# Kernel optimization log

Measured on AMD Instinct MI355X. Metric: run time of the kernel, lower is better.

Reference implementation:

```python
import jax, jax.numpy as jnp
import numpy as np

N = 50000
E = 800000
D = 256   # output_channel_dim
K = 32
L = 4     # num_of_layers


def setup_inputs() -> dict:
    key = jax.random.key(0)
    ks = jax.random.split(key, 10)
    x = jax.random.normal(ks[0], (N, 1), dtype=jnp.float32)
    edge_index = jax.random.randint(ks[1], (2, E), 0, N, dtype=jnp.int64)
    edge_attr = jax.random.uniform(ks[2], (E,), dtype=jnp.float32)
    # GGNN per-layer propagation weights (L, D, D)
    weight = jax.random.normal(ks[3], (L, D, D), dtype=jnp.float32) / np.sqrt(D)
    # GRUCell params (torch layout: [r|z|n] stacked along first dim)
    w_ih = jax.random.normal(ks[4], (3 * D, D), dtype=jnp.float32) / np.sqrt(D)
    w_hh = jax.random.normal(ks[5], (3 * D, D), dtype=jnp.float32) / np.sqrt(D)
    b_ih = jax.random.normal(ks[6], (3 * D,), dtype=jnp.float32) * 0.01
    b_hh = jax.random.normal(ks[7], (3 * D,), dtype=jnp.float32) * 0.01
    # readout Linear(D, K)
    w_ro = jax.random.normal(ks[8], (D, K), dtype=jnp.float32) / np.sqrt(D)
    b_ro = jax.random.normal(ks[9], (K,), dtype=jnp.float32) * 0.01
    return {"x": x, "edge_index": edge_index, "edge_attr": edge_attr,
            "weight": weight, "w_ih": w_ih, "w_hh": w_hh,
            "b_ih": b_ih, "b_hh": b_hh, "w_ro": w_ro, "b_ro": b_ro}


def _gru_cell(m, h, w_ih, w_hh, b_ih, b_hh):
    # torch.nn.GRUCell math; gates stacked [r|z|n]
    gi = m @ w_ih.T + b_ih   # (N, 3D)
    gh = h @ w_hh.T + b_hh   # (N, 3D)
    i_r, i_z, i_n = jnp.split(gi, 3, axis=-1)
    h_r, h_z, h_n = jnp.split(gh, 3, axis=-1)
    r = jax.nn.sigmoid(i_r + h_r)
    z = jax.nn.sigmoid(i_z + h_z)
    n = jnp.tanh(i_n + r * h_n)
    return (1.0 - z) * n + z * h


def reference(x, edge_index, edge_attr, weight, w_ih, w_hh, b_ih, b_hh, w_ro, b_ro):
    src, dst = edge_index[0], edge_index[1]
    n_nodes, d = x.shape[0], weight.shape[-1]
    # pad input features with zeros up to out_channels
    h = jnp.concatenate([x, jnp.zeros((n_nodes, d - x.shape[-1]), x.dtype)], axis=-1)
    for i in range(weight.shape[0]):
        m = h @ weight[i]                                    # (N, D)
        msg = edge_attr[:, None] * m[src]                    # (E, D)
        agg = jax.ops.segment_sum(msg, dst, num_segments=n_nodes)  # (N, D)
        h = _gru_cell(agg, h, w_ih, w_hh, b_ih, b_hh)
    logits = h @ w_ro + b_ro                                 # (N, K)
    return jax.nn.softmax(logits, axis=-1)
```

## Files before the change

### kernel.cpp

```cpp
#include <hip/hip_runtime.h>

#define D 256
#define K_OUT 32
#define L_LAYERS 4
#define NPAD 50048

typedef __attribute__((ext_vector_type(8))) short bf16x8;
typedef __attribute__((ext_vector_type(4))) float f32x4;
typedef __attribute__((address_space(3))) unsigned int lds_u32;
typedef const __attribute__((address_space(1))) unsigned int glb_u32;

__device__ __forceinline__ float sigm(float v) { return 1.f / (1.f + __expf(-v)); }
__device__ __forceinline__ unsigned short f2bf(float f) {
    unsigned u = __float_as_uint(f);
    u = u + 0x7fffu + ((u >> 16) & 1u);
    return (unsigned short)(u >> 16);
}
__device__ __forceinline__ float bf2f(unsigned short s) {
    return __uint_as_float(((unsigned)s) << 16);
}
__device__ __forceinline__ void gload16(const unsigned short* g, unsigned short* l) {
    __builtin_amdgcn_global_load_lds((glb_u32*)g, (lds_u32*)l, 16, 0, 0);
}

__global__ __launch_bounds__(256) void hist_kernel(const int* __restrict__ dst,
                                                   int* __restrict__ cnt, int E) {
    int idx = blockIdx.x * blockDim.x + threadIdx.x;
    for (int e = idx; e < E; e += gridDim.x * blockDim.x)
        atomicAdd(&cnt[dst[e]], 1);
}

__global__ __launch_bounds__(1024) void scan_kernel(const int* __restrict__ cnt,
                                                    int* __restrict__ rowptr,
                                                    int* __restrict__ cursor, int n) {
    __shared__ int sdata[1024];
    int t = threadIdx.x;
    int chunk = (n + 1023) / 1024;
    int start = t * chunk;
    int end = start + chunk; if (end > n) end = n;
    int s = 0;
    for (int i = start; i < end; i++) s += cnt[i];
    sdata[t] = s;
    __syncthreads();
    for (int off = 1; off < 1024; off <<= 1) {
        int v = (t >= off) ? sdata[t - off] : 0;
        __syncthreads();
        sdata[t] += v;
        __syncthreads();
    }
    int base = sdata[t] - s;
    for (int i = start; i < end; i++) {
        rowptr[i] = base;
        cursor[i] = base;
        base += cnt[i];
    }
    if (end == n && start <= n) rowptr[n] = base;
}

__global__ __launch_bounds__(256) void reorder_kernel(const int* __restrict__ src,
                                                      const int* __restrict__ dst,
                                                      const float* __restrict__ ea,
                                                      int* __restrict__ cursor,
                                                      int* __restrict__ esrc,
                                                      float* __restrict__ eval, int E) {
    int idx = blockIdx.x * blockDim.x + threadIdx.x;
    for (int e = idx; e < E; e += gridDim.x * blockDim.x) {
        int slot = atomicAdd(&cursor[dst[e]], 1);
        esrc[slot] = src[e];
        eval[slot] = ea[e];
    }
}

__global__ __launch_bounds__(256) void prep_wih_kernel(const float* __restrict__ weight,
                                                       const float* __restrict__ w_ih,
                                                       float* __restrict__ P) {
    int l = blockIdx.z;
    const float* A = weight + (size_t)l * D * D;
    float* Cdst = P + (size_t)l * 256 * 768;
    __shared__ float As[32][64 + 4];
    __shared__ float Bs[32][64 + 4];
    int tid = threadIdx.x;
    int tx = tid & 15, ty = tid >> 4;
    int bk = blockIdx.x * 64;
    int bn = blockIdx.y * 64;
    float acc[4][4] = {};
    for (int jb = 0; jb < D; jb += 32) {
        #pragma unroll
        for (int i = 0; i < 2; i++) {
            int lin = tid + i * 256;
            int row = lin >> 3;
            int c4 = (lin & 7) << 2;
            float4 v = *(const float4*)&A[(size_t)(bk + row) * D + jb + c4];
            As[c4+0][row]=v.x; As[c4+1][row]=v.y; As[c4+2][row]=v.z; As[c4+3][row]=v.w;
            float4 w = *(const float4*)&w_ih[(size_t)(bn + row) * D + jb + c4];
            Bs[c4+0][row]=w.x; Bs[c4+1][row]=w.y; Bs[c4+2][row]=w.z; Bs[c4+3][row]=w.w;
        }
        __syncthreads();
        #pragma unroll
        for (int jj = 0; jj < 32; jj++) {
            float a[4], b[4];
            *(float4*)a = *(const float4*)&As[jj][ty*4];
            *(float4*)b = *(const float4*)&Bs[jj][tx*4];
            #pragma unroll
            for (int i = 0; i < 4; i++)
                #pragma unroll
                for (int j = 0; j < 4; j++)
                    acc[i][j] += a[i] * b[j];
        }
        __syncthreads();
    }
    #pragma unroll
    for (int i = 0; i < 4; i++)
        *(float4*)&Cdst[(size_t)(bk + ty*4 + i) * 768 + bn + tx*4] =
            make_float4(acc[i][0], acc[i][1], acc[i][2], acc[i][3]);
}

__global__ __launch_bounds__(256) void pack_bt2_kernel(const float* __restrict__ P,
                                                       const float* __restrict__ w_hh,
                                                       unsigned short* __restrict__ BT2) {
    long long idx = (long long)blockIdx.x * 256 + threadIdx.x;
    int l = (int)(idx >> 20);
    int rem = (int)(idx & 1048575);
    int c = rem >> 10;
    int k2 = rem & 1023;
    int g = c >> 8, d = c & 255;
    int k = k2 & 511;
    float val;
    if (k < 256) {
        val = (g == 0) ? P[(size_t)l * 196608 + (size_t)k * 768 + d]
            : (g == 1) ? P[(size_t)l * 196608 + (size_t)k * 768 + 256 + d]
            : (g == 2) ? P[(size_t)l * 196608 + (size_t)k * 768 + 512 + d]
            : 0.f;
    } else {
        int kk = k - 256;
        val = (g == 0) ? w_hh[(size_t)d * D + kk]
            : (g == 1) ? w_hh[(size_t)(256 + d) * D + kk]
            : (g == 3) ? w_hh[(size_t)(512 + d) * D + kk]
            : 0.f;
    }
    unsigned short hi = f2bf(val);
    BT2[idx] = (k2 < 512) ? hi : f2bf(val - bf2f(hi));
}

__global__ __launch_bounds__(256) void sgather_kernel(const float* __restrict__ x,
                                                      const int* __restrict__ rowptr,
                                                      const int* __restrict__ esrc,
                                                      const float* __restrict__ eval,
                                                      float* __restrict__ sx, int n) {
    int node = blockIdx.x * blockDim.x + threadIdx.x;
    if (node >= n) return;
    float s = 0.f;
    int end = rowptr[node + 1];
    for (int e = rowptr[node]; e < end; e++) s += eval[e] * x[esrc[e]];
    sx[node] = s;
}

__global__ __launch_bounds__(256) void layer0_kernel(const float* __restrict__ x,
                                                     const float* __restrict__ sx,
                                                     const float* __restrict__ P0,
                                                     const float* __restrict__ w_hh,
                                                     const float* __restrict__ b_ih,
                                                     const float* __restrict__ b_hh,
                                                     float* __restrict__ hout, int M) {
    int node = blockIdx.x * 4 + (threadIdx.x >> 6);
    if (node >= M) return;
    int d0 = (threadIdx.x & 63) * 4;
    float sxn = sx[node], xn = x[node];
    float4 r0 = *(const float4*)&P0[d0];
    float4 z0 = *(const float4*)&P0[256 + d0];
    float4 n0 = *(const float4*)&P0[512 + d0];
    float r1[4], z1[4], n1[4];
    #pragma unroll
    for (int j = 0; j < 4; j++) {
        r1[j] = w_hh[(size_t)(d0 + j) * D];
        z1[j] = w_hh[(size_t)(256 + d0 + j) * D];
        n1[j] = w_hh[(size_t)(512 + d0 + j) * D];
    }
    float4 bir = *(const float4*)&b_ih[d0];
    float4 biz = *(const float4*)&b_ih[256 + d0];
    float4 bin = *(const float4*)&b_ih[512 + d0];
    float4 bhr = *(const float4*)&b_hh[d0];
    float4 bhz = *(const float4*)&b_hh[256 + d0];
    float4 bhn = *(const float4*)&b_hh[512 + d0];
    float rr[4] = {sxn*r0.x + xn*r1[0] + bir.x + bhr.x, sxn*r0.y + xn*r1[1] + bir.y + bhr.y,
                   sxn*r0.z + xn*r1[2] + bir.z + bhr.z, sxn*r0.w + xn*r1[3] + bir.w + bhr.w};
    float zz[4] = {sxn*z0.x + xn*z1[0] + biz.x + bhz.x, sxn*z0.y + xn*z1[1] + biz.y + bhz.y,
                   sxn*z0.z + xn*z1[2] + biz.z + bhz.z, sxn*z0.w + xn*z1[3] + biz.w + bhz.w};
    float ni[4] = {sxn*n0.x + bin.x, sxn*n0.y + bin.y, sxn*n0.z + bin.z, sxn*n0.w + bin.w};
    float nh[4] = {xn*n1[0] + bhn.x, xn*n1[1] + bhn.y, xn*n1[2] + bhn.z, xn*n1[3] + bhn.w};
    float o[4];
    #pragma unroll
    for (int j = 0; j < 4; j++) {
        float r = sigm(rr[j]);
        float z = sigm(zz[j]);
        float nn = tanhf(ni[j] + r * nh[j]);
        float hp = (d0 + j == 0) ? xn : 0.f;
        o[j] = (1.f - z) * nn + z * hp;
    }
    *(float4*)&hout[(size_t)node * D + d0] = make_float4(o[0], o[1], o[2], o[3]);
}

__global__ __launch_bounds__(256) void gather_bf_kernel(const float* __restrict__ h,
                                                        const int* __restrict__ rowptr,
                                                        const int* __restrict__ esrc,
                                                        const float* __restrict__ eval,
                                                        unsigned short* __restrict__ A2, int n) {
    int node = (blockIdx.x * 256 + threadIdx.x) >> 6;
    int lane = threadIdx.x & 63;
    if (node >= n) return;
    int beg = rowptr[node], end = rowptr[node + 1];
    float4 acc = make_float4(0.f, 0.f, 0.f, 0.f);
    for (int e = beg; e < end; e++) {
        int s = esrc[e];
        float a = eval[e];
        float4 v = *(const float4*)&h[(size_t)s * D + lane * 4];
        acc.x += a * v.x; acc.y += a * v.y; acc.z += a * v.z; acc.w += a * v.w;
    }
    ushort4 hi = make_ushort4(f2bf(acc.x), f2bf(acc.y), f2bf(acc.z), f2bf(acc.w));
    ushort4 lo = make_ushort4(f2bf(acc.x - bf2f(hi.x)), f2bf(acc.y - bf2f(hi.y)),
                              f2bf(acc.z - bf2f(hi.z)), f2bf(acc.w - bf2f(hi.w)));
    *(ushort4*)&A2[(size_t)node * 1024 + lane * 4] = hi;
    *(ushort4*)&A2[(size_t)node * 1024 + 512 + lane * 4] = lo;
    float4 hv = *(const float4*)&h[(size_t)node * D + lane * 4];
    ushort4 hh = make_ushort4(f2bf(hv.x), f2bf(hv.y), f2bf(hv.z), f2bf(hv.w));
    ushort4 hl = make_ushort4(f2bf(hv.x - bf2f(hh.x)), f2bf(hv.y - bf2f(hh.y)),
                              f2bf(hv.z - bf2f(hh.z)), f2bf(hv.w - bf2f(hh.w)));
    *(ushort4*)&A2[(size_t)node * 1024 + 256 + lane * 4] = hh;
    *(ushort4*)&A2[(size_t)node * 1024 + 768 + lane * 4] = hl;
}

__global__ __launch_bounds__(256, 2) void gru_mfma_kernel(const unsigned short* __restrict__ A2,
                                                          const unsigned short* __restrict__ BT2,
                                                          const float* __restrict__ b_ih,
                                                          const float* __restrict__ b_hh,
                                                          float* __restrict__ h, int M) {
    __shared__ unsigned short sm[24576];
    int tid = threadIdx.x;
    int lane = tid & 63;
    int wid = tid >> 6;
    int wr = wid >> 1, wc = wid & 1;
    int bm = blockIdx.x * 128;
    int bnd = blockIdx.y * 64;

    unsigned goff[12];
    bool gisA[12];
    #pragma unroll
    for (int ff = 0; ff < 12; ff++) {
        int f = wid * 12 + ff;
        unsigned r, cb;
        bool isA = (f < 16);
        if (f < 8)       { r = bm + f * 16 + (lane & 15);       cb = 0; }
        else if (f < 16) { r = bm + (f - 8) * 16 + (lane & 15); cb = 512; }
        else if (f < 32) { int q = f - 16; r = (q >> 2) * 256 + bnd + (q & 3) * 16 + (lane & 15); cb = 0; }
        else             { int q = f - 32; r = (q >> 2) * 256 + bnd + (q & 3) * 16 + (lane & 15); cb = 512; }
        goff[ff] = r * 1024u + cb + ((lane >> 4) << 3);
        gisA[ff] = isA;
    }

    f32x4 acc[4][8];
    #pragma unroll
    for (int i = 0; i < 4; i++)
        #pragma unroll
        for (int j = 0; j < 8; j++)
            acc[i][j] = (f32x4){0.f, 0.f, 0.f, 0.f};

    for (int c = 0; c < 16; c++) {
        #pragma unroll
        for (int ff = 0; ff < 12; ff++) {
            const unsigned short* g = (gisA[ff] ? A2 : BT2) + goff[ff] + c * 32;
            gload16(g, &sm[(wid * 12 + ff) * 512]);
        }
        __syncthreads();
        bf16x8 ah[4], al[4], bh[8], bl[8];
        #pragma unroll
        for (int m = 0; m < 4; m++) {
            ah[m] = *(const bf16x8*)&sm[(wr * 4 + m) * 512 + lane * 8];
            al[m] = *(const bf16x8*)&sm[(8 + wr * 4 + m) * 512 + lane * 8];
        }
        #pragma unroll
        for (int n = 0; n < 8; n++) {
            int fb = (n >> 1) * 4 + wc * 2 + (n & 1);
            bh[n] = *(const bf16x8*)&sm[(16 + fb) * 512 + lane * 8];
            bl[n] = *(const bf16x8*)&sm[(32 + fb) * 512 + lane * 8];
        }
        #pragma unroll
        for (int m = 0; m < 4; m++)
            #pragma unroll
            for (int n = 0; n < 8; n++) {
                acc[m][n] = __builtin_amdgcn_mfma_f32_16x16x32_bf16(ah[m], bh[n], acc[m][n], 0, 0, 0);
                acc[m][n] = __builtin_amdgcn_mfma_f32_16x16x32_bf16(al[m], bh[n], acc[m][n], 0, 0, 0);
                acc[m][n] = __builtin_amdgcn_mfma_f32_16x16x32_bf16(ah[m], bl[n], acc[m][n], 0, 0, 0);
            }
        __syncthreads();
    }

    int dbase = bnd + wc * 32 + (lane & 15);
    int rbase = bm + wr * 64 + ((lane >> 4) << 2);
    #pragma unroll
    for (int j = 0; j < 2; j++) {
        int d = dbase + j * 16;
        float cbr = b_ih[d] + b_hh[d];
        float cbz = b_ih[D + d] + b_hh[D + d];
        float bin = b_ih[2 * D + d];
        float bhn = b_hh[2 * D + d];
        #pragma unroll
        for (int m = 0; m < 4; m++) {
            #pragma unroll
            for (int q = 0; q < 4; q++) {
                int row = rbase + m * 16 + q;
                if (row < M) {
                    float r = sigm(acc[m][j][q] + cbr);
                    float z = sigm(acc[m][2 + j][q] + cbz);
                    float nn = tanhf(acc[m][4 + j][q] + bin + r * (acc[m][6 + j][q] + bhn));
                    float* hp = &h[(size_t)row * D + d];
                    float hv = *hp;
                    *hp = (1.f - z) * nn + z * hv;
                }
            }
        }
    }
}

__global__ __launch_bounds__(256) void readout_kernel(const float* __restrict__ h,
                                                      const float* __restrict__ w_ro,
                                                      const float* __restrict__ b_ro,
                                                      float* __restrict__ out, int M) {
    __shared__ float ws_[D * K_OUT];
    for (int i = threadIdx.x; i < D * K_OUT; i += 256) ws_[i] = w_ro[i];
    __syncthreads();
    int group = threadIdx.x >> 5;
    int col   = threadIdx.x & 31;
    int node  = blockIdx.x * 8 + group;
    if (node >= M) return;
    float acc = b_ro[col];
    const float* hrow = &h[(size_t)node * D];
    #pragma unroll 8
    for (int k = 0; k < D; k++) acc += hrow[k] * ws_[k * K_OUT + col];
    float mx = acc;
    #pragma unroll
    for (int off = 16; off > 0; off >>= 1) mx = fmaxf(mx, __shfl_xor(mx, off, 32));
    float e = __expf(acc - mx);
    float s = e;
    #pragma unroll
    for (int off = 16; off > 0; off >>= 1) s += __shfl_xor(s, off, 32);
    out[(size_t)node * K_OUT + col] = e / s;
}

extern "C" void kernel_launch(void* const* d_in, const int* in_sizes, int n_in,
                              void* d_out, int out_size, void* d_ws, size_t ws_size,
                              hipStream_t stream) {
    const float* x      = (const float*)d_in[0];
    const int*   ei     = (const int*)d_in[1];
    const float* ea     = (const float*)d_in[2];
    const float* weight = (const float*)d_in[3];
    const float* w_ih   = (const float*)d_in[4];
    const float* w_hh   = (const float*)d_in[5];
    const float* b_ih   = (const float*)d_in[6];
    const float* b_hh   = (const float*)d_in[7];
    const float* w_ro   = (const float*)d_in[8];
    const float* b_ro   = (const float*)d_in[9];
    float* out = (float*)d_out;

    int N = in_sizes[0];
    int E = in_sizes[2];
    const int* src = ei;
    const int* dst = ei + E;

    size_t ND = (size_t)N * D;
    float* h = (float*)d_ws;
    unsigned short* A2 = (unsigned short*)(h + ND);
    float* P = (float*)(A2 + (size_t)NPAD * 1024);
    unsigned short* BT2 = (unsigned short*)(P + (size_t)L_LAYERS * 256 * 768);
    float* sx = (float*)(BT2 + (size_t)L_LAYERS * 1024 * 1024);
    int* cnt = (int*)(sx + N);
    int* rowptr = cnt + (N + 1);
    int* cursor = rowptr + (N + 1);
    int* esrc = cursor + (N + 1);
    float* eval = (float*)(esrc + E);

    hipMemsetAsync(cnt, 0, (N + 1) * sizeof(int), stream);
    hist_kernel<<<1024, 256, 0, stream>>>(dst, cnt, E);
    scan_kernel<<<1, 1024, 0, stream>>>(cnt, rowptr, cursor, N);
    reorder_kernel<<<1024, 256, 0, stream>>>(src, dst, ea, cursor, esrc, eval, E);

    prep_wih_kernel<<<dim3(4, 12, 4), 256, 0, stream>>>(weight, w_ih, P);
    pack_bt2_kernel<<<16384, 256, 0, stream>>>(P, w_hh, BT2);

    sgather_kernel<<<(N + 255) / 256, 256, 0, stream>>>(x, rowptr, esrc, eval, sx, N);
    layer0_kernel<<<(N + 3) / 4, 256, 0, stream>>>(x, sx, P, w_hh, b_ih, b_hh, h, N);

    dim3 gm(NPAD / 128, 4);
    int gather_blocks = (N * 64 + 255) / 256;
    for (int l = 1; l < L_LAYERS; l++) {
        gather_bf_kernel<<<gather_blocks, 256, 0, stream>>>(h, rowptr, esrc, eval, A2, N);
        gru_mfma_kernel<<<gm, 256, 0, stream>>>(A2, BT2 + (size_t)l * 1024 * 1024,
                                                b_ih, b_hh, h, N);
    }
    readout_kernel<<<(N + 7) / 8, 256, 0, stream>>>(h, w_ro, b_ro, out, N);
}
```

Baseline: 1.605 ms.

## Double-buffer GRU GEMM LDS tiles and skip zero blocks of n-gate weights

The GRU MFMA kernel now double-buffers its LDS tiles, prefetching the next K-chunk while computing the current one, and drops one of the two barriers per iteration. It also exploits the block structure of the concatenated [agg|h] weight matrix: for the n gate, the first half of K uses only the input-side weights and the second half only the hidden-side weights. So it loads 6 instead of 8 B fragments per chunk and issues a quarter fewer MFMAs. LDS per block grows (2x20480 shorts), which could affect occupancy at launch bounds of 2.

After: 1.478 ms. 7.9% less time.

```diff
diff --git a/kernel.cpp b/kernel.cpp
--- a/kernel.cpp
+++ b/kernel.cpp
@@ -234,7 +234,7 @@
                                                           const float* __restrict__ b_ih,
                                                           const float* __restrict__ b_hh,
                                                           float* __restrict__ h, int M) {
-    __shared__ unsigned short sm[24576];
+    __shared__ unsigned short sm[2][20480];
     int tid = threadIdx.x;
     int lane = tid & 63;
     int wid = tid >> 6;
@@ -242,19 +242,21 @@
     int bm = blockIdx.x * 128;
     int bnd = blockIdx.y * 64;
 
-    unsigned goff[12];
-    bool gisA[12];
-    #pragma unroll
-    for (int ff = 0; ff < 12; ff++) {
-        int f = wid * 12 + ff;
-        unsigned r, cb;
-        bool isA = (f < 16);
-        if (f < 8)       { r = bm + f * 16 + (lane & 15);       cb = 0; }
-        else if (f < 16) { r = bm + (f - 8) * 16 + (lane & 15); cb = 512; }
-        else if (f < 32) { int q = f - 16; r = (q >> 2) * 256 + bnd + (q & 3) * 16 + (lane & 15); cb = 0; }
-        else             { int q = f - 32; r = (q >> 2) * 256 + bnd + (q & 3) * 16 + (lane & 15); cb = 512; }
-        goff[ff] = r * 1024u + cb + ((lane >> 4) << 3);
-        gisA[ff] = isA;
+    unsigned gbase[10];
+    bool gA[10], gG2[10];
+    #pragma unroll
+    for (int ff = 0; ff < 10; ff++) {
+        int f = wid * 10 + ff;
+        unsigned row, cb;
+        bool isA, isG2 = false;
+        if (f < 8)       { row = bm + f * 16 + (lane & 15);        cb = 0;   isA = true; }
+        else if (f < 16) { row = bm + (f - 8) * 16 + (lane & 15);  cb = 512; isA = true; }
+        else if (f < 28) { int q = f - 16; int gs = q >> 2; int df = q & 3;
+                           row = gs * 256 + bnd + df * 16 + (lane & 15); cb = 0; isA = false; isG2 = (gs == 2); }
+        else             { int q = f - 28; int gs = q >> 2; int df = q & 3;
+                           row = gs * 256 + bnd + df * 16 + (lane & 15); cb = 512; isA = false; isG2 = (gs == 2); }
+        gbase[ff] = row * 1024u + cb + ((lane >> 4) << 3);
+        gA[ff] = isA; gG2[ff] = isG2;
     }
 
     f32x4 acc[4][8];
@@ -264,41 +266,58 @@
         for (int j = 0; j < 8; j++)
             acc[i][j] = (f32x4){0.f, 0.f, 0.f, 0.f};
 
-    for (int c = 0; c < 16; c++) {
-        #pragma unroll
-        for (int ff = 0; ff < 12; ff++) {
-            const unsigned short* g = (gisA[ff] ? A2 : BT2) + goff[ff] + c * 32;
-            gload16(g, &sm[(wid * 12 + ff) * 512]);
-        }
-        __syncthreads();
-        bf16x8 ah[4], al[4], bh[8], bl[8];
-        #pragma unroll
-        for (int m = 0; m < 4; m++) {
-            ah[m] = *(const bf16x8*)&sm[(wr * 4 + m) * 512 + lane * 8];
-            al[m] = *(const bf16x8*)&sm[(8 + wr * 4 + m) * 512 + lane * 8];
-        }
-        #pragma unroll
-        for (int n = 0; n < 8; n++) {
-            int fb = (n >> 1) * 4 + wc * 2 + (n & 1);
-            bh[n] = *(const bf16x8*)&sm[(16 + fb) * 512 + lane * 8];
-            bl[n] = *(const bf16x8*)&sm[(32 + fb) * 512 + lane * 8];
-        }
-        #pragma unroll
-        for (int m = 0; m < 4; m++)
-            #pragma unroll
-            for (int n = 0; n < 8; n++) {
-                acc[m][n] = __builtin_amdgcn_mfma_f32_16x16x32_bf16(ah[m], bh[n], acc[m][n], 0, 0, 0);
-                acc[m][n] = __builtin_amdgcn_mfma_f32_16x16x32_bf16(al[m], bh[n], acc[m][n], 0, 0, 0);
-                acc[m][n] = __builtin_amdgcn_mfma_f32_16x16x32_bf16(ah[m], bl[n], acc[m][n], 0, 0, 0);
-            }
-        __syncthreads();
-    }
-
-    int dbase = bnd + wc * 32 + (lane & 15);
+#define STAGE(C_, B_)                                                              \
+    {                                                                              \
+        _Pragma("unroll")                                                          \
+        for (int ff = 0; ff < 10; ff++) {                                          \
+            const unsigned short* gp = (gA[ff] ? A2 : BT2) + gbase[ff]             \
+                + (C_) * 32 + ((gG2[ff] && (C_) >= 8) ? 262144u : 0u);             \
+            gload16(gp, &sm[B_][(wid * 10 + ff) * 512]);                           \
+        }                                                                          \
+    }
+
+#define KBODY(C_, NIOFF_)                                                          \
+    {                                                                              \
+        int cur = (C_) & 1;                                                        \
+        if ((C_) < 15) STAGE((C_) + 1, cur ^ 1);                                   \
+        bf16x8 ah[4], al[4], bh[6], bl[6];                                         \
+        _Pragma("unroll")                                                          \
+        for (int m = 0; m < 4; m++) {                                              \
+            ah[m] = *(const bf16x8*)&sm[cur][(wr * 4 + m) * 512 + lane * 8];       \
+            al[m] = *(const bf16x8*)&sm[cur][(8 + wr * 4 + m) * 512 + lane * 8];   \
+        }                                                                          \
+        _Pragma("unroll")                                                          \
+        for (int j = 0; j < 6; j++) {                                              \
+            int fb = 16 + (j >> 1) * 4 + wc * 2 + (j & 1);                         \
+            bh[j] = *(const bf16x8*)&sm[cur][fb * 512 + lane * 8];                 \
+            bl[j] = *(const bf16x8*)&sm[cur][(fb + 12) * 512 + lane * 8];          \
+        }                                                                          \
+        _Pragma("unroll")                                                          \
+        for (int m = 0; m < 4; m++) {                                              \
+            _Pragma("unroll")                                                      \
+            for (int j = 0; j < 6; j++) {                                          \
+                int na = (j < 4) ? j : (NIOFF_) + (j & 1);                         \
+                acc[m][na] = __builtin_amdgcn_mfma_f32_16x16x32_bf16(ah[m], bh[j], acc[m][na], 0, 0, 0); \
+                acc[m][na] = __builtin_amdgcn_mfma_f32_16x16x32_bf16(al[m], bh[j], acc[m][na], 0, 0, 0); \
+                acc[m][na] = __builtin_amdgcn_mfma_f32_16x16x32_bf16(ah[m], bl[j], acc[m][na], 0, 0, 0); \
+            }                                                                      \
+        }                                                                          \
+        __syncthreads();                                                           \
+    }
+
+    STAGE(0, 0);
+    __syncthreads();
+    #pragma unroll
+    for (int cc = 0; cc < 8; cc++) KBODY(cc, 4)
+    #pragma unroll
+    for (int cc = 8; cc < 16; cc++) KBODY(cc, 6)
+#undef STAGE
+#undef KBODY
+
     int rbase = bm + wr * 64 + ((lane >> 4) << 2);
     #pragma unroll
-    for (int j = 0; j < 2; j++) {
-        int d = dbase + j * 16;
+    for (int jj = 0; jj < 2; jj++) {
+        int d = bnd + (wc * 2 + jj) * 16 + (lane & 15);
         float cbr = b_ih[d] + b_hh[d];
         float cbz = b_ih[D + d] + b_hh[D + d];
         float bin = b_ih[2 * D + d];
@@ -309,9 +328,9 @@
             for (int q = 0; q < 4; q++) {
                 int row = rbase + m * 16 + q;
                 if (row < M) {
-                    float r = sigm(acc[m][j][q] + cbr);
-                    float z = sigm(acc[m][2 + j][q] + cbz);
-                    float nn = tanhf(acc[m][4 + j][q] + bin + r * (acc[m][6 + j][q] + bhn));
+                    float r = sigm(acc[m][jj][q] + cbr);
+                    float z = sigm(acc[m][2 + jj][q] + cbz);
+                    float nn = tanhf(acc[m][4 + jj][q] + bin + r * (acc[m][6 + jj][q] + bhn));
                     float* hp = &h[(size_t)row * D + d];
                     float hv = *hp;
                     *hp = (1.f - z) * nn + z * hv;
```
